# Optimization experiments

Hardware: AMD Instinct MI355X
Metric: run time of the kernel (lower is better)

Reference implementation:

```python
import jax, jax.numpy as jnp
import numpy as np

B, N, K, D = 16, 8192, 20, 64  # batch, points, neighbors, feature dim
LN_EPS = 1e-5


def setup_inputs() -> dict:
    key = jax.random.key(0)
    k1, k2, k3 = jax.random.split(key, 3)
    x = jax.random.normal(k1, (B, N, D), dtype=jnp.float32)
    neighbor_ind = jax.random.randint(k2, (B, N, K), 0, N)
    # torch Linear(2D -> D, bias=False): weight shape (out=D, in=2D), y = feat @ W.T
    W = jax.random.normal(k3, (D, 2 * D), dtype=jnp.float32) * (1.0 / np.sqrt(2 * D))
    gamma = jnp.ones((D,), jnp.float32)
    beta = jnp.zeros((D,), jnp.float32)
    return {"x": x, "neighbor_ind": neighbor_ind, "W": W, "gamma": gamma, "beta": beta}


def reference(x, neighbor_ind, W, gamma, beta):
    # route(): gather neighbor features and build [neighbor - center, center]
    neighbor_x = jax.vmap(lambda xb, ib: xb[ib])(x, neighbor_ind)        # (b, n, k, d)
    center = x[:, :, None, :]                                            # (b, n, 1, d)
    feat = jnp.concatenate(
        [neighbor_x - center, jnp.broadcast_to(center, neighbor_x.shape)], axis=-1
    )                                                                    # (b, n, k, 2d)
    # per-edge Linear (bias=False), then max over k neighbors
    h = jnp.einsum('bnke,oe->bnko', feat, W)                             # (b, n, k, d)
    h = h.max(axis=2)                                                    # (b, n, d)
    # LayerNorm over last dim, then exact GELU
    mu = h.mean(axis=-1, keepdims=True)
    var = jnp.mean((h - mu) ** 2, axis=-1, keepdims=True)
    hn = (h - mu) * jax.lax.rsqrt(var + LN_EPS) * gamma + beta
    return jax.nn.gelu(hn, approximate=False)
```

## Files before the change

### kernel.cpp

```cpp
#include <hip/hip_runtime.h>
#include <math.h>

#define B_ 16
#define N_ 8192
#define K_ 20
#define NPTS (B_ * N_)

typedef __attribute__((ext_vector_type(4))) float f4;
typedef __attribute__((ext_vector_type(8))) short s8;
typedef __attribute__((ext_vector_type(4))) unsigned int u4;
typedef __attribute__((ext_vector_type(4))) unsigned short us4;

__device__ __forceinline__ unsigned short f2bf(float f) {
    union { float f; unsigned u; } v; v.f = f;
    return (unsigned short)((v.u + 0x7FFFu + ((v.u >> 16) & 1u)) >> 16);
}
__device__ __forceinline__ float bfhi(unsigned w) { return __uint_as_float(w & 0xFFFF0000u); }
__device__ __forceinline__ float bflo(unsigned w) { return __uint_as_float(w << 16); }

__global__ __launch_bounds__(256) void prep_kernel(const float* __restrict__ W,
                                                   unsigned short* __restrict__ Wg) {
    const int i = blockIdx.x * 256 + threadIdx.x;
    const int j = i >> 6, d = i & 63;
    const float v = (j < 64) ? W[j * 128 + d]
                             : (W[(j - 64) * 128 + 64 + d] - W[(j - 64) * 128 + d]);
    Wg[i] = f2bf(v);
}

__global__ __launch_bounds__(256) void proj_kernel(const float* __restrict__ x,
                                                   const unsigned short* __restrict__ Wg,
                                                   unsigned short* __restrict__ Y1,
                                                   unsigned short* __restrict__ Bs) {
    __shared__ unsigned short Wl[128 * 72];
    const int t = threadIdx.x;

    for (int i = t; i < 1024; i += 256) {
        u4 v = ((const u4*)Wg)[i];
        *((u4*)((char*)Wl + (i >> 3) * 144 + (i & 7) * 16)) = v;
    }
    __syncthreads();

    const int lane = t & 63;
    const int wv = t >> 6;
    const int m = lane & 15;
    const int q = lane >> 4;
    const int pbase = blockIdx.x * 64 + wv * 16;

    const float* xr = x + (size_t)(pbase + m) * 64 + q * 8;
    f4 x0 = *(const f4*)(xr);
    f4 x1 = *(const f4*)(xr + 4);
    f4 x2 = *(const f4*)(xr + 32);
    f4 x3 = *(const f4*)(xr + 36);
    s8 X0, X1;
    X0[0]=(short)f2bf(x0.x); X0[1]=(short)f2bf(x0.y); X0[2]=(short)f2bf(x0.z); X0[3]=(short)f2bf(x0.w);
    X0[4]=(short)f2bf(x1.x); X0[5]=(short)f2bf(x1.y); X0[6]=(short)f2bf(x1.z); X0[7]=(short)f2bf(x1.w);
    X1[0]=(short)f2bf(x2.x); X1[1]=(short)f2bf(x2.y); X1[2]=(short)f2bf(x2.z); X1[3]=(short)f2bf(x2.w);
    X1[4]=(short)f2bf(x3.x); X1[5]=(short)f2bf(x3.y); X1[6]=(short)f2bf(x3.z); X1[7]=(short)f2bf(x3.w);

    f4 acc[8];
#pragma unroll
    for (int tt = 0; tt < 8; ++tt) acc[tt] = (f4)0.f;

#pragma unroll
    for (int s = 0; s < 2; ++s) {
        const s8 X = s ? X1 : X0;
#pragma unroll
        for (int tt = 0; tt < 8; ++tt) {
            s8 w = *(const s8*)((const char*)Wl + (16 * tt + m) * 144 + s * 64 + q * 16);
            acc[tt] = __builtin_amdgcn_mfma_f32_16x16x32_bf16(w, X, acc[tt], 0, 0, 0);
        }
    }

    const size_t prow = (size_t)(pbase + m) * 64;
#pragma unroll
    for (int tt = 0; tt < 4; ++tt) {
        us4 u;
        u.x = f2bf(acc[tt][0]); u.y = f2bf(acc[tt][1]);
        u.z = f2bf(acc[tt][2]); u.w = f2bf(acc[tt][3]);
        *(us4*)&Y1[prow + tt * 16 + q * 4] = u;
    }
#pragma unroll
    for (int tt = 4; tt < 8; ++tt) {
        us4 u;
        u.x = f2bf(acc[tt][0]); u.y = f2bf(acc[tt][1]);
        u.z = f2bf(acc[tt][2]); u.w = f2bf(acc[tt][3]);
        *(us4*)&Bs[prow + (tt - 4) * 16 + q * 4] = u;
    }
}

__global__ __launch_bounds__(256) void gather_kernel(const unsigned short* __restrict__ Y1,
                                                     const unsigned short* __restrict__ Bs,
                                                     const int* __restrict__ ind,
                                                     const float* __restrict__ gamma,
                                                     const float* __restrict__ beta,
                                                     float* __restrict__ out) {
    const int lane = threadIdx.x & 63;
    const int wave = threadIdx.x >> 6;
    const int sub = lane & 7;
    const int q = lane >> 3;
    const int bi = blockIdx.x;
    const int bt = bi & 15;
    const int jj = bi >> 4;
    const int p = bt * N_ + jj * 32 + wave * 8 + q;
    const int bbase = bt * N_ * 64;

    int idxs[K_];
    const int4* ip = (const int4*)&ind[p * K_];
#pragma unroll
    for (int v = 0; v < 5; ++v) {
        int4 iv = ip[v];
        idxs[4 * v + 0] = iv.x; idxs[4 * v + 1] = iv.y;
        idxs[4 * v + 2] = iv.z; idxs[4 * v + 3] = iv.w;
    }

    f4 ma = (f4)(-INFINITY), mb = (f4)(-INFINITY);
#pragma unroll
    for (int r = 0; r < 2; ++r) {
        u4 rv[10];
#pragma unroll
        for (int k = 0; k < 10; ++k)
            rv[k] = *(const u4*)(Y1 + bbase + idxs[r * 10 + k] * 64 + sub * 8);
#pragma unroll
        for (int k = 0; k < 10; ++k) {
            ma.x = fmaxf(ma.x, bflo(rv[k].x)); ma.y = fmaxf(ma.y, bfhi(rv[k].x));
            ma.z = fmaxf(ma.z, bflo(rv[k].y)); ma.w = fmaxf(ma.w, bfhi(rv[k].y));
            mb.x = fmaxf(mb.x, bflo(rv[k].z)); mb.y = fmaxf(mb.y, bfhi(rv[k].z));
            mb.z = fmaxf(mb.z, bflo(rv[k].w)); mb.w = fmaxf(mb.w, bfhi(rv[k].w));
        }
    }

    u4 bsv = __builtin_nontemporal_load((const u4*)(Bs + (size_t)p * 64 + sub * 8));
    f4 ha, hb;
    ha.x = ma.x + bflo(bsv.x); ha.y = ma.y + bfhi(bsv.x);
    ha.z = ma.z + bflo(bsv.y); ha.w = ma.w + bfhi(bsv.y);
    hb.x = mb.x + bflo(bsv.z); hb.y = mb.y + bfhi(bsv.z);
    hb.z = mb.z + bflo(bsv.w); hb.w = mb.w + bfhi(bsv.w);

    float s = ha.x + ha.y + ha.z + ha.w + hb.x + hb.y + hb.z + hb.w;
#pragma unroll
    for (int off = 4; off >= 1; off >>= 1) s += __shfl_xor(s, off, 64);
    const float mu = s * (1.0f / 64.0f);
    f4 da = ha - mu, db = hb - mu;
    float v2 = da.x * da.x + da.y * da.y + da.z * da.z + da.w * da.w
             + db.x * db.x + db.y * db.y + db.z * db.z + db.w * db.w;
#pragma unroll
    for (int off = 4; off >= 1; off >>= 1) v2 += __shfl_xor(v2, off, 64);
    const float rstd = rsqrtf(v2 * (1.0f / 64.0f) + 1e-5f);

    const f4 g0 = *(const f4*)&gamma[sub * 8];
    const f4 g1 = *(const f4*)&gamma[sub * 8 + 4];
    const f4 b0 = *(const f4*)&beta[sub * 8];
    const f4 b1 = *(const f4*)&beta[sub * 8 + 4];
    f4 na = da * rstd * g0 + b0;
    f4 nb = db * rstd * g1 + b1;

    f4 r0, r1;
    r0.x = 0.5f * na.x * (1.0f + erff(na.x * 0.70710678f));
    r0.y = 0.5f * na.y * (1.0f + erff(na.y * 0.70710678f));
    r0.z = 0.5f * na.z * (1.0f + erff(na.z * 0.70710678f));
    r0.w = 0.5f * na.w * (1.0f + erff(na.w * 0.70710678f));
    r1.x = 0.5f * nb.x * (1.0f + erff(nb.x * 0.70710678f));
    r1.y = 0.5f * nb.y * (1.0f + erff(nb.y * 0.70710678f));
    r1.z = 0.5f * nb.z * (1.0f + erff(nb.z * 0.70710678f));
    r1.w = 0.5f * nb.w * (1.0f + erff(nb.w * 0.70710678f));
    float* op = &out[(size_t)p * 64 + sub * 8];
    __builtin_nontemporal_store(r0, (f4*)op);
    __builtin_nontemporal_store(r1, (f4*)(op + 4));
}

extern "C" void kernel_launch(void* const* d_in, const int* in_sizes, int n_in,
                              void* d_out, int out_size, void* d_ws, size_t ws_size,
                              hipStream_t stream) {
    const float* x     = (const float*)d_in[0];
    const int*   ind   = (const int*)d_in[1];
    const float* W     = (const float*)d_in[2];
    const float* gamma = (const float*)d_in[3];
    const float* beta  = (const float*)d_in[4];
    float* out = (float*)d_out;

    unsigned short* Bs = (unsigned short*)d_ws;
    unsigned short* Y1 = Bs + (size_t)NPTS * 64;
    unsigned short* Wg = Y1 + (size_t)NPTS * 64;

    prep_kernel<<<32, 256, 0, stream>>>(W, Wg);
    proj_kernel<<<NPTS / 64, 256, 0, stream>>>(x, Wg, Y1, Bs);
    gather_kernel<<<NPTS / 32, 256, 0, stream>>>(Y1, Bs, ind, gamma, beta, out);
}
```

Measured before the change: 131.7 us.

## Fuse prep, projection and gather into one persistent kernel with grid barrier

Merges the three kernels into a single persistent launch of 512 blocks. Each block builds the bf16 weight tile in shared memory, projects four 64-point tiles, waits at a software grid-wide barrier made of an atomic counter and a flag, then gathers and normalizes 256 points. Blocks are mapped to batches by XCD index so each batch's Y1 stays within one XCD's L2. The aim is to remove launch gaps and the separate weight-prep pass. The risks are barrier spin cost, a possible deadlock if not all 512 blocks are resident at once, and a hipMemsetAsync added on every call.

```diff
diff --git a/kernel.cpp b/kernel.cpp
--- a/kernel.cpp
+++ b/kernel.cpp
@@ -5,6 +5,7 @@
 #define N_ 8192
 #define K_ 20
 #define NPTS (B_ * N_)
+#define NBLK 512
 
 typedef __attribute__((ext_vector_type(4))) float f4;
 typedef __attribute__((ext_vector_type(8))) short s8;
@@ -18,25 +19,25 @@
 __device__ __forceinline__ float bfhi(unsigned w) { return __uint_as_float(w & 0xFFFF0000u); }
 __device__ __forceinline__ float bflo(unsigned w) { return __uint_as_float(w << 16); }
 
-__global__ __launch_bounds__(256) void prep_kernel(const float* __restrict__ W,
-                                                   unsigned short* __restrict__ Wg) {
-    const int i = blockIdx.x * 256 + threadIdx.x;
-    const int j = i >> 6, d = i & 63;
-    const float v = (j < 64) ? W[j * 128 + d]
-                             : (W[(j - 64) * 128 + 64 + d] - W[(j - 64) * 128 + d]);
-    Wg[i] = f2bf(v);
-}
-
-__global__ __launch_bounds__(256) void proj_kernel(const float* __restrict__ x,
-                                                   const unsigned short* __restrict__ Wg,
-                                                   unsigned short* __restrict__ Y1,
-                                                   unsigned short* __restrict__ Bs) {
+__global__ __launch_bounds__(256, 2) void fused_kernel(
+        const float* __restrict__ x, const int* __restrict__ ind,
+        const float* __restrict__ W, const float* __restrict__ gamma,
+        const float* __restrict__ beta, float* __restrict__ out,
+        unsigned short* __restrict__ Y1, unsigned short* __restrict__ Bs,
+        unsigned* __restrict__ bar_cnt, unsigned* __restrict__ bar_flag) {
     __shared__ unsigned short Wl[128 * 72];
     const int t = threadIdx.x;
+    const int bx = blockIdx.x;
+    const int xcd = bx & 7;
+    const int lb = bx >> 3;
+    const int bt = 2 * xcd + (lb >> 5);
+    const int w = lb & 31;
 
-    for (int i = t; i < 1024; i += 256) {
-        u4 v = ((const u4*)Wg)[i];
-        *((u4*)((char*)Wl + (i >> 3) * 144 + (i & 7) * 16)) = v;
+    for (int i = t; i < 8192; i += 256) {
+        const int j = i >> 6, d = i & 63;
+        const float v = (j < 64) ? W[j * 128 + d]
+                                 : (W[(j - 64) * 128 + 64 + d] - W[(j - 64) * 128 + d]);
+        Wl[j * 72 + d] = f2bf(v);
     }
     __syncthreads();
 
@@ -44,128 +45,138 @@
     const int wv = t >> 6;
     const int m = lane & 15;
     const int q = lane >> 4;
-    const int pbase = blockIdx.x * 64 + wv * 16;
 
-    const float* xr = x + (size_t)(pbase + m) * 64 + q * 8;
-    f4 x0 = *(const f4*)(xr);
-    f4 x1 = *(const f4*)(xr + 4);
-    f4 x2 = *(const f4*)(xr + 32);
-    f4 x3 = *(const f4*)(xr + 36);
-    s8 X0, X1;
-    X0[0]=(short)f2bf(x0.x); X0[1]=(short)f2bf(x0.y); X0[2]=(short)f2bf(x0.z); X0[3]=(short)f2bf(x0.w);
-    X0[4]=(short)f2bf(x1.x); X0[5]=(short)f2bf(x1.y); X0[6]=(short)f2bf(x1.z); X0[7]=(short)f2bf(x1.w);
-    X1[0]=(short)f2bf(x2.x); X1[1]=(short)f2bf(x2.y); X1[2]=(short)f2bf(x2.z); X1[3]=(short)f2bf(x2.w);
-    X1[4]=(short)f2bf(x3.x); X1[5]=(short)f2bf(x3.y); X1[6]=(short)f2bf(x3.z); X1[7]=(short)f2bf(x3.w);
+#pragma unroll 1
+    for (int tl = 0; tl < 4; ++tl) {
+        const int pbase = bt * N_ + (w * 4 + tl) * 64 + wv * 16;
 
-    f4 acc[8];
+        const float* xr = x + (size_t)(pbase + m) * 64 + q * 8;
+        f4 x0 = *(const f4*)(xr);
+        f4 x1 = *(const f4*)(xr + 4);
+        f4 x2 = *(const f4*)(xr + 32);
+        f4 x3 = *(const f4*)(xr + 36);
+        s8 X0, X1;
+        X0[0]=(short)f2bf(x0.x); X0[1]=(short)f2bf(x0.y); X0[2]=(short)f2bf(x0.z); X0[3]=(short)f2bf(x0.w);
+        X0[4]=(short)f2bf(x1.x); X0[5]=(short)f2bf(x1.y); X0[6]=(short)f2bf(x1.z); X0[7]=(short)f2bf(x1.w);
+        X1[0]=(short)f2bf(x2.x); X1[1]=(short)f2bf(x2.y); X1[2]=(short)f2bf(x2.z); X1[3]=(short)f2bf(x2.w);
+        X1[4]=(short)f2bf(x3.x); X1[5]=(short)f2bf(x3.y); X1[6]=(short)f2bf(x3.z); X1[7]=(short)f2bf(x3.w);
+
+        f4 acc[8];
 #pragma unroll
-    for (int tt = 0; tt < 8; ++tt) acc[tt] = (f4)0.f;
-
+        for (int tt = 0; tt < 8; ++tt) acc[tt] = (f4)0.f;
 #pragma unroll
-    for (int s = 0; s < 2; ++s) {
-        const s8 X = s ? X1 : X0;
+        for (int s = 0; s < 2; ++s) {
+            const s8 X = s ? X1 : X0;
 #pragma unroll
-        for (int tt = 0; tt < 8; ++tt) {
-            s8 w = *(const s8*)((const char*)Wl + (16 * tt + m) * 144 + s * 64 + q * 16);
-            acc[tt] = __builtin_amdgcn_mfma_f32_16x16x32_bf16(w, X, acc[tt], 0, 0, 0);
+            for (int tt = 0; tt < 8; ++tt) {
+                s8 wf = *(const s8*)((const char*)Wl + (16 * tt + m) * 144 + s * 64 + q * 16);
+                acc[tt] = __builtin_amdgcn_mfma_f32_16x16x32_bf16(wf, X, acc[tt], 0, 0, 0);
+            }
+        }
+        const size_t prow = (size_t)(pbase + m) * 64;
+#pragma unroll
+        for (int tt = 0; tt < 4; ++tt) {
+            us4 u;
+            u.x = f2bf(acc[tt][0]); u.y = f2bf(acc[tt][1]);
+            u.z = f2bf(acc[tt][2]); u.w = f2bf(acc[tt][3]);
+            *(us4*)&Y1[prow + tt * 16 + q * 4] = u;
+        }
+#pragma unroll
+        for (int tt = 4; tt < 8; ++tt) {
+            us4 u;
+            u.x = f2bf(acc[tt][0]); u.y = f2bf(acc[tt][1]);
+            u.z = f2bf(acc[tt][2]); u.w = f2bf(acc[tt][3]);
+            *(us4*)&Bs[prow + (tt - 4) * 16 + q * 4] = u;
         }
     }
 
-    const size_t prow = (size_t)(pbase + m) * 64;
+    __syncthreads();
+    if (t == 0) {
+        __threadfence();
+        unsigned old = atomicAdd(bar_cnt, 1u);
+        if (old == (unsigned)(NBLK - 1)) {
+            atomicExch(bar_flag, 1u);
+        } else {
+            long guard = 0;
+            while (__hip_atomic_load(bar_flag, __ATOMIC_ACQUIRE, __HIP_MEMORY_SCOPE_AGENT) == 0u) {
+                __builtin_amdgcn_s_sleep(4);
+                if (++guard > 200000000L) break;
+            }
+        }
+        __threadfence();
+    }
+    __syncthreads();
+
+    const int sub = lane & 7;
+    const int q2 = lane >> 3;
+    const int bbase = bt * N_ * 64;
+#pragma unroll 1
+    for (int it = 0; it < 8; ++it) {
+        const int p = bt * N_ + w * 256 + it * 32 + wv * 8 + q2;
+
+        int idxs[K_];
+        const int4* ip = (const int4*)&ind[p * K_];
 #pragma unroll
-    for (int tt = 0; tt < 4; ++tt) {
-        us4 u;
-        u.x = f2bf(acc[tt][0]); u.y = f2bf(acc[tt][1]);
-        u.z = f2bf(acc[tt][2]); u.w = f2bf(acc[tt][3]);
-        *(us4*)&Y1[prow + tt * 16 + q * 4] = u;
+        for (int v = 0; v < 5; ++v) {
+            int4 iv = ip[v];
+            idxs[4 * v + 0] = iv.x; idxs[4 * v + 1] = iv.y;
+            idxs[4 * v + 2] = iv.z; idxs[4 * v + 3] = iv.w;
+        }
+
+        f4 ma = (f4)(-INFINITY), mb = (f4)(-INFINITY);
+#pragma unroll
+        for (int r = 0; r < 2; ++r) {
+            u4 rv[10];
+#pragma unroll
+            for (int k = 0; k < 10; ++k)
+                rv[k] = *(const u4*)(Y1 + bbase + idxs[r * 10 + k] * 64 + sub * 8);
+#pragma unroll
+            for (int k = 0; k < 10; ++k) {
+                ma.x = fmaxf(ma.x, bflo(rv[k].x)); ma.y = fmaxf(ma.y, bfhi(rv[k].x));
+                ma.z = fmaxf(ma.z, bflo(rv[k].y)); ma.w = fmaxf(ma.w, bfhi(rv[k].y));
+                mb.x = fmaxf(mb.x, bflo(rv[k].z)); mb.y = fmaxf(mb.y, bfhi(rv[k].z));
+                mb.z = fmaxf(mb.z, bflo(rv[k].w)); mb.w = fmaxf(mb.w, bfhi(rv[k].w));
+            }
+        }
+
+        u4 bsv = *(const u4*)(Bs + (size_t)p * 64 + sub * 8);
+        f4 ha, hb;
+        ha.x = ma.x + bflo(bsv.x); ha.y = ma.y + bfhi(bsv.x);
+        ha.z = ma.z + bflo(bsv.y); ha.w = ma.w + bfhi(bsv.y);
+        hb.x = mb.x + bflo(bsv.z); hb.y = mb.y + bfhi(bsv.z);
+        hb.z = mb.z + bflo(bsv.w); hb.w = mb.w + bfhi(bsv.w);
+
+        float s = ha.x + ha.y + ha.z + ha.w + hb.x + hb.y + hb.z + hb.w;
+#pragma unroll
+        for (int off = 4; off >= 1; off >>= 1) s += __shfl_xor(s, off, 64);
+        const float mu = s * (1.0f / 64.0f);
+        f4 da = ha - mu, db = hb - mu;
+        float v2 = da.x * da.x + da.y * da.y + da.z * da.z + da.w * da.w
+                 + db.x * db.x + db.y * db.y + db.z * db.z + db.w * db.w;
+#pragma unroll
+        for (int off = 4; off >= 1; off >>= 1) v2 += __shfl_xor(v2, off, 64);
+        const float rstd = rsqrtf(v2 * (1.0f / 64.0f) + 1e-5f);
+
+        const f4 g0 = *(const f4*)&gamma[sub * 8];
+        const f4 g1 = *(const f4*)&gamma[sub * 8 + 4];
+        const f4 b0 = *(const f4*)&beta[sub * 8];
+        const f4 b1 = *(const f4*)&beta[sub * 8 + 4];
+        f4 na = da * rstd * g0 + b0;
+        f4 nb = db * rstd * g1 + b1;
+
+        f4 r0, r1;
+        r0.x = 0.5f * na.x * (1.0f + erff(na.x * 0.70710678f));
+        r0.y = 0.5f * na.y * (1.0f + erff(na.y * 0.70710678f));
+        r0.z = 0.5f * na.z * (1.0f + erff(na.z * 0.70710678f));
+        r0.w = 0.5f * na.w * (1.0f + erff(na.w * 0.70710678f));
+        r1.x = 0.5f * nb.x * (1.0f + erff(nb.x * 0.70710678f));
+        r1.y = 0.5f * nb.y * (1.0f + erff(nb.y * 0.70710678f));
+        r1.z = 0.5f * nb.z * (1.0f + erff(nb.z * 0.70710678f));
+        r1.w = 0.5f * nb.w * (1.0f + erff(nb.w * 0.70710678f));
+        float* op = &out[(size_t)p * 64 + sub * 8];
+        __builtin_nontemporal_store(r0, (f4*)op);
+        __builtin_nontemporal_store(r1, (f4*)(op + 4));
     }
-#pragma unroll
-    for (int tt = 4; tt < 8; ++tt) {
-        us4 u;
-        u.x = f2bf(acc[tt][0]); u.y = f2bf(acc[tt][1]);
-        u.z = f2bf(acc[tt][2]); u.w = f2bf(acc[tt][3]);
-        *(us4*)&Bs[prow + (tt - 4) * 16 + q * 4] = u;
-    }
-}
-
-__global__ __launch_bounds__(256) void gather_kernel(const unsigned short* __restrict__ Y1,
-                                                     const unsigned short* __restrict__ Bs,
-                                                     const int* __restrict__ ind,
-                                                     const float* __restrict__ gamma,
-                                                     const float* __restrict__ beta,
-                                                     float* __restrict__ out) {
-    const int lane = threadIdx.x & 63;
-    const int wave = threadIdx.x >> 6;
-    const int sub = lane & 7;
-    const int q = lane >> 3;
-    const int bi = blockIdx.x;
-    const int bt = bi & 15;
-    const int jj = bi >> 4;
-    const int p = bt * N_ + jj * 32 + wave * 8 + q;
-    const int bbase = bt * N_ * 64;
-
-    int idxs[K_];
-    const int4* ip = (const int4*)&ind[p * K_];
-#pragma unroll
-    for (int v = 0; v < 5; ++v) {
-        int4 iv = ip[v];
-        idxs[4 * v + 0] = iv.x; idxs[4 * v + 1] = iv.y;
-        idxs[4 * v + 2] = iv.z; idxs[4 * v + 3] = iv.w;
-    }
-
-    f4 ma = (f4)(-INFINITY), mb = (f4)(-INFINITY);
-#pragma unroll
-    for (int r = 0; r < 2; ++r) {
-        u4 rv[10];
-#pragma unroll
-        for (int k = 0; k < 10; ++k)
-            rv[k] = *(const u4*)(Y1 + bbase + idxs[r * 10 + k] * 64 + sub * 8);
-#pragma unroll
-        for (int k = 0; k < 10; ++k) {
-            ma.x = fmaxf(ma.x, bflo(rv[k].x)); ma.y = fmaxf(ma.y, bfhi(rv[k].x));
-            ma.z = fmaxf(ma.z, bflo(rv[k].y)); ma.w = fmaxf(ma.w, bfhi(rv[k].y));
-            mb.x = fmaxf(mb.x, bflo(rv[k].z)); mb.y = fmaxf(mb.y, bfhi(rv[k].z));
-            mb.z = fmaxf(mb.z, bflo(rv[k].w)); mb.w = fmaxf(mb.w, bfhi(rv[k].w));
-        }
-    }
-
-    u4 bsv = __builtin_nontemporal_load((const u4*)(Bs + (size_t)p * 64 + sub * 8));
-    f4 ha, hb;
-    ha.x = ma.x + bflo(bsv.x); ha.y = ma.y + bfhi(bsv.x);
-    ha.z = ma.z + bflo(bsv.y); ha.w = ma.w + bfhi(bsv.y);
-    hb.x = mb.x + bflo(bsv.z); hb.y = mb.y + bfhi(bsv.z);
-    hb.z = mb.z + bflo(bsv.w); hb.w = mb.w + bfhi(bsv.w);
-
-    float s = ha.x + ha.y + ha.z + ha.w + hb.x + hb.y + hb.z + hb.w;
-#pragma unroll
-    for (int off = 4; off >= 1; off >>= 1) s += __shfl_xor(s, off, 64);
-    const float mu = s * (1.0f / 64.0f);
-    f4 da = ha - mu, db = hb - mu;
-    float v2 = da.x * da.x + da.y * da.y + da.z * da.z + da.w * da.w
-             + db.x * db.x + db.y * db.y + db.z * db.z + db.w * db.w;
-#pragma unroll
-    for (int off = 4; off >= 1; off >>= 1) v2 += __shfl_xor(v2, off, 64);
-    const float rstd = rsqrtf(v2 * (1.0f / 64.0f) + 1e-5f);
-
-    const f4 g0 = *(const f4*)&gamma[sub * 8];
-    const f4 g1 = *(const f4*)&gamma[sub * 8 + 4];
-    const f4 b0 = *(const f4*)&beta[sub * 8];
-    const f4 b1 = *(const f4*)&beta[sub * 8 + 4];
-    f4 na = da * rstd * g0 + b0;
-    f4 nb = db * rstd * g1 + b1;
-
-    f4 r0, r1;
-    r0.x = 0.5f * na.x * (1.0f + erff(na.x * 0.70710678f));
-    r0.y = 0.5f * na.y * (1.0f + erff(na.y * 0.70710678f));
-    r0.z = 0.5f * na.z * (1.0f + erff(na.z * 0.70710678f));
-    r0.w = 0.5f * na.w * (1.0f + erff(na.w * 0.70710678f));
-    r1.x = 0.5f * nb.x * (1.0f + erff(nb.x * 0.70710678f));
-    r1.y = 0.5f * nb.y * (1.0f + erff(nb.y * 0.70710678f));
-    r1.z = 0.5f * nb.z * (1.0f + erff(nb.z * 0.70710678f));
-    r1.w = 0.5f * nb.w * (1.0f + erff(nb.w * 0.70710678f));
-    float* op = &out[(size_t)p * 64 + sub * 8];
-    __builtin_nontemporal_store(r0, (f4*)op);
-    __builtin_nontemporal_store(r1, (f4*)(op + 4));
 }
 
 extern "C" void kernel_launch(void* const* d_in, const int* in_sizes, int n_in,
@@ -180,9 +191,9 @@
 
     unsigned short* Bs = (unsigned short*)d_ws;
     unsigned short* Y1 = Bs + (size_t)NPTS * 64;
-    unsigned short* Wg = Y1 + (size_t)NPTS * 64;
+    unsigned* bar = (unsigned*)((char*)d_ws + (size_t)NPTS * 64 * 4);
 
-    prep_kernel<<<32, 256, 0, stream>>>(W, Wg);
-    proj_kernel<<<NPTS / 64, 256, 0, stream>>>(x, Wg, Y1, Bs);
-    gather_kernel<<<NPTS / 32, 256, 0, stream>>>(Y1, Bs, ind, gamma, beta, out);
+    hipMemsetAsync(bar, 0, 8, stream);
+    fused_kernel<<<NBLK, 256, 0, stream>>>(x, ind, W, gamma, beta, out, Y1, Bs,
+                                           bar, bar + 1);
 }
```

New measurement: 228.2 us. +73.3%, slower.

## Schedule gather tiles per XCC via atomic work queue for L2 locality

Applied to the files above, without the earlier changes.

Replaces the static block-to-tile mapping in the gather kernel with a dynamic scheduler. Each block reads its XCC id and claims tiles from a per-XCC batch range through atomics, then steals from a global counter once its range is exhausted. The aim is to keep each batch's Y1 rows resident in one XCC's L2 so that random neighbor gathers hit cache. It adds a memset, per-block atomics, and twice as many launched blocks, half of which exit immediately.

```diff
diff --git a/kernel.cpp b/kernel.cpp
--- a/kernel.cpp
+++ b/kernel.cpp
@@ -5,6 +5,8 @@
 #define N_ 8192
 #define K_ 20
 #define NPTS (B_ * N_)
+#define NTILE 4096
+#define TPG 512
 
 typedef __attribute__((ext_vector_type(4))) float f4;
 typedef __attribute__((ext_vector_type(8))) short s8;
@@ -60,14 +62,13 @@
     f4 acc[8];
 #pragma unroll
     for (int tt = 0; tt < 8; ++tt) acc[tt] = (f4)0.f;
-
 #pragma unroll
     for (int s = 0; s < 2; ++s) {
         const s8 X = s ? X1 : X0;
 #pragma unroll
         for (int tt = 0; tt < 8; ++tt) {
-            s8 w = *(const s8*)((const char*)Wl + (16 * tt + m) * 144 + s * 64 + q * 16);
-            acc[tt] = __builtin_amdgcn_mfma_f32_16x16x32_bf16(w, X, acc[tt], 0, 0, 0);
+            s8 wf = *(const s8*)((const char*)Wl + (16 * tt + m) * 144 + s * 64 + q * 16);
+            acc[tt] = __builtin_amdgcn_mfma_f32_16x16x32_bf16(wf, X, acc[tt], 0, 0, 0);
         }
     }
 
@@ -88,19 +89,19 @@
     }
 }
 
-__global__ __launch_bounds__(256) void gather_kernel(const unsigned short* __restrict__ Y1,
-                                                     const unsigned short* __restrict__ Bs,
-                                                     const int* __restrict__ ind,
-                                                     const float* __restrict__ gamma,
-                                                     const float* __restrict__ beta,
-                                                     float* __restrict__ out) {
+__device__ __forceinline__ void gather_tile(int tile,
+                                            const unsigned short* __restrict__ Y1,
+                                            const unsigned short* __restrict__ Bs,
+                                            const int* __restrict__ ind,
+                                            const float* __restrict__ gamma,
+                                            const float* __restrict__ beta,
+                                            float* __restrict__ out) {
     const int lane = threadIdx.x & 63;
     const int wave = threadIdx.x >> 6;
     const int sub = lane & 7;
     const int q = lane >> 3;
-    const int bi = blockIdx.x;
-    const int bt = bi & 15;
-    const int jj = bi >> 4;
+    const int bt = tile >> 8;
+    const int jj = tile & 255;
     const int p = bt * N_ + jj * 32 + wave * 8 + q;
     const int bbase = bt * N_ * 64;
 
@@ -168,6 +169,48 @@
     __builtin_nontemporal_store(r1, (f4*)(op + 4));
 }
 
+#define HWREG_XCC_ID_IMM (20 | (31 << 11))
+
+__global__ __launch_bounds__(256) void gather_kernel(const unsigned short* __restrict__ Y1,
+                                                     const unsigned short* __restrict__ Bs,
+                                                     const int* __restrict__ ind,
+                                                     const float* __restrict__ gamma,
+                                                     const float* __restrict__ beta,
+                                                     float* __restrict__ out,
+                                                     unsigned* __restrict__ cnt,
+                                                     unsigned* __restrict__ cntg,
+                                                     unsigned* __restrict__ flags)
+{
+    __shared__ int tile_s;
+    const int g = (int)(__builtin_amdgcn_s_getreg(HWREG_XCC_ID_IMM) & 7u);
+
+    for (;;) {
+        if (threadIdx.x == 0) {
+            int tile = -1;
+            for (;;) {
+                unsigned t = atomicAdd(&cnt[g], 1u);
+                if (t >= TPG) break;
+                int cand = g * TPG + (int)t;
+                if (atomicCAS(&flags[cand], 0u, 1u) == 0u) { tile = cand; break; }
+            }
+            if (tile < 0) {
+                for (;;) {
+                    unsigned t = atomicAdd(cntg, 1u);
+                    if (t >= NTILE) break;
+                    if (atomicCAS(&flags[t], 0u, 1u) == 0u) { tile = (int)t; break; }
+                }
+            }
+            tile_s = tile;
+        }
+        __syncthreads();
+        const int tile = tile_s;
+        __syncthreads();
+        if (tile < 0) return;
+        gather_tile(tile, Y1, Bs, ind, gamma, beta, out);
+        return;
+    }
+}
+
 extern "C" void kernel_launch(void* const* d_in, const int* in_sizes, int n_in,
                               void* d_out, int out_size, void* d_ws, size_t ws_size,
                               hipStream_t stream) {
@@ -181,8 +224,14 @@
     unsigned short* Bs = (unsigned short*)d_ws;
     unsigned short* Y1 = Bs + (size_t)NPTS * 64;
     unsigned short* Wg = Y1 + (size_t)NPTS * 64;
-
+    unsigned* sched = (unsigned*)(Wg + 8192);
+    unsigned* cnt   = sched;
+    unsigned* cntg  = sched + 8;
+    unsigned* flags = sched + 16;
+
+    hipMemsetAsync(sched, 0, (16 + NTILE) * sizeof(unsigned), stream);
     prep_kernel<<<32, 256, 0, stream>>>(W, Wg);
     proj_kernel<<<NPTS / 64, 256, 0, stream>>>(x, Wg, Y1, Bs);
-    gather_kernel<<<NPTS / 32, 256, 0, stream>>>(Y1, Bs, ind, gamma, beta, out);
-}
+    gather_kernel<<<2 * NTILE, 256, 0, stream>>>(Y1, Bs, ind, gamma, beta, out,
+                                                 cnt, cntg, flags);
+}
```

Result: slower. 298.0 us (+126.3%).
